# Performance work log

Measured on AMD Instinct MI355X. Metric: run time of the kernel, lower is better.

Reference implementation:

```python
import jax, jax.numpy as jnp
import numpy as np

NUM_HEADS = 8
TEMPERATURE = 10000.0


def sine_embed(pos, dim):
    """Sine positional embedding of 2D offsets. pos [..., 2] -> [..., dim]."""
    half = dim // 2  # dims per coordinate
    dim_t = TEMPERATURE ** (2.0 * (jnp.arange(half) // 2).astype(jnp.float32) / half)
    s = pos[..., :, None] / dim_t  # [..., 2, half]
    emb = jnp.stack([jnp.sin(s[..., 0::2]), jnp.cos(s[..., 1::2])], axis=-1)
    emb = emb.reshape(s.shape[:-1] + (half,))  # interleaved sin/cos per coord
    return emb.reshape(pos.shape[:-1] + (dim,))


def setup_inputs() -> dict:
    key = jax.random.key(0)
    ks = jax.random.split(key, 16)
    N, H, W, C, K = 2, 40, 40, 256, 100
    h = NUM_HEADS
    sc = 1.0 / np.sqrt(C)
    return {
        "query_feature": jax.random.normal(ks[0], (N, H, W, C), jnp.float32),
        "query_position": jax.random.uniform(ks[1], (N, H, W, 2), jnp.float32),
        "key_feature": jax.random.normal(ks[2], (N, K, C), jnp.float32),
        "key_position": jax.random.uniform(ks[3], (N, K, 2), jnp.float32),
        # MultiheadAttention params (torch convention: weight [out, in])
        "in_proj_w": jax.random.normal(ks[4], (3 * C, C), jnp.float32) * sc,
        "in_proj_b": jnp.zeros((3 * C,), jnp.float32),
        "out_proj_w": jax.random.normal(ks[5], (C, C), jnp.float32) * sc,
        "out_proj_b": jnp.zeros((C,), jnp.float32),
        # PositionalEncodingSineLearned MLP: sine(C) -> C -> num_heads
        "pos_w1": jax.random.normal(ks[6], (C, C), jnp.float32) * sc,
        "pos_b1": jnp.zeros((C,), jnp.float32),
        "pos_w2": jax.random.normal(ks[7], (h, C), jnp.float32) * sc,
        "pos_b2": jnp.zeros((h,), jnp.float32),
        # cat_pos branch params
        "pos_trans_w": jax.random.normal(ks[8], (2, 2), jnp.float32),
        "embed_w": jax.random.normal(ks[9], (C, C + 2), jnp.float32) * 0.01,
        "embed_b": jnp.zeros((C,), jnp.float32),
    }


def reference(query_feature, query_position, key_feature, key_position,
              in_proj_w, in_proj_b, out_proj_w, out_proj_b,
              pos_w1, pos_b1, pos_w2, pos_b2,
              pos_trans_w, embed_w, embed_b):
    N, H, W, C = query_feature.shape
    h = NUM_HEADS
    d = C // h
    q = query_feature.reshape(N, -1, C)            # [N,Q,C]
    qp = query_position.reshape(N, -1, 2)          # [N,Q,2] (scale_terms = 1.0)
    Q = q.shape[1]
    K = key_feature.shape[1]

    # pairwise relative positions: [N,Q,K,2]
    rel_pos = key_position[:, None, :, :] - qp[:, :, None, :]

    # learned sine relative positional encoding -> per-head additive bias
    pe = sine_embed(rel_pos, C)                              # [N,Q,K,C]
    hid = jax.nn.relu(pe @ pos_w1.T + pos_b1)                # [N,Q,K,C]
    bias = (hid @ pos_w2.T + pos_b2).transpose(0, 3, 1, 2)   # [N,h,Q,K]

    # multihead attention with additive relative bias
    wq, wk, wv = jnp.split(in_proj_w, 3, axis=0)
    bq, bk, bv = jnp.split(in_proj_b, 3, axis=0)
    qh = ((q @ wq.T + bq).reshape(N, Q, h, d)) * (d ** -0.5)
    kh = (key_feature @ wk.T + bk).reshape(N, K, h, d)
    vh = (key_feature @ wv.T + bv).reshape(N, K, h, d)
    scores = jnp.einsum('nqhd,nkhd->nhqk', qh, kh) + bias
    attn = jax.nn.softmax(scores, axis=-1)                   # [N,h,Q,K]
    ctx = jnp.einsum('nhqk,nkhd->nqhd', attn, vh).reshape(N, Q, C)
    refined = ctx @ out_proj_w.T + out_proj_b                # [N,Q,C]

    # cat_pos: attention-weighted relative position aggregation
    attn_w = attn.mean(axis=1)                               # [N,Q,K]
    new_rel = jnp.einsum('nqk,nqkc->nqc', attn_w, jax.lax.stop_gradient(rel_pos))
    new_pos = new_rel @ pos_trans_w.T                        # [N,Q,2]

    feat = jax.nn.relu(q + refined)
    feat = jax.nn.relu(jnp.concatenate([feat, new_pos], axis=-1) @ embed_w.T + embed_b)
    return feat.reshape(N, H, W, C)
```

## Files before the change

kernel.cpp:

```cpp
#include <hip/hip_runtime.h>
#include <math.h>

typedef __bf16 bf16x8 __attribute__((ext_vector_type(8)));
typedef __bf16 bf16x4 __attribute__((ext_vector_type(4)));
typedef float  f32x4  __attribute__((ext_vector_type(4)));

#define WS_KH    0u
#define WS_VH    51200u
#define WS_EWT   102400u
#define WS_OWT   168448u
#define WS_QHB   233984u
#define WS_BIASB 643584u
#define WS_KEB   1923584u
#define WS_W1B   1949984u
#define WS_W2PB  1982752u
#define WS_IPWT  1984800u

__device__ __forceinline__ float rdlane(float v, int l) {
  return __uint_as_float(__builtin_amdgcn_readlane(__float_as_uint(v), l));
}

__global__ __launch_bounds__(256) void prep1_kernel(
    const float* __restrict__ kpos,
    const float* __restrict__ pos_w1, const float* __restrict__ pos_w2,
    const float* __restrict__ embed_w, const float* __restrict__ out_w,
    const float* __restrict__ ipw, float* __restrict__ ws)
{
  __shared__ float tile[64 * 65];
  int bid = blockIdx.x, t = threadIdx.x;

  if (bid < 50) {
    int r = bid * 4 + (t >> 6);
    int u = t & 63;
    float p0 = kpos[r * 2 + 0], p1 = kpos[r * 2 + 1];
    __bf16* keb = (__bf16*)(ws + WS_KEB);
    bf16x4 o;
#pragma unroll
    for (int j = 0; j < 4; j++) {
      int col = u * 4 + j;
      int c = col >> 7, i = (col & 127) >> 1;
      float p = c ? p1 : p0;
      float inv = exp2f((float)i * (-13.287712379549449f / 64.0f));
      float v = p * inv;
      o[j] = (__bf16)((col & 1) ? __cosf(v) : __sinf(v));
    }
    *(bf16x4*)(keb + r * 264 + u * 4) = o;
  } else if (bid < 114) {
    int idx = (bid - 50) * 1024 + t * 4;
    float4 v = *(const float4*)(pos_w1 + idx);
    bf16x4 o; o[0] = (__bf16)v.x; o[1] = (__bf16)v.y; o[2] = (__bf16)v.z; o[3] = (__bf16)v.w;
    *(bf16x4*)((__bf16*)(ws + WS_W1B) + idx) = o;
  } else if (bid == 114) {
    __bf16* w2pb = (__bf16*)(ws + WS_W2PB);
    for (int i = 0; i < 16; i++) {
      int idx = t * 16 + i;
      w2pb[idx] = (idx < 2048) ? (__bf16)pos_w2[idx] : (__bf16)0.0f;
    }
  } else if (bid < 135) {
    int idx = bid - 115;
    int j0 = (idx / 4) * 64, c0 = (idx % 4) * 64;
    int jj = t & 63, rq = t >> 6;
    for (int rr = 0; rr < 16; rr++) {
      int c = rr * 4 + rq;
      float v = (j0 + jj < 258) ? embed_w[(c0 + c) * 258 + j0 + jj] : 0.0f;
      tile[c * 65 + jj] = v;
    }
    __syncthreads();
    int cc = t & 63, jq = t >> 6;
    for (int pp = 0; pp < 16; pp++) {
      int j = pp * 4 + jq;
      if (j0 + j < 258)
        ws[WS_EWT + (unsigned)(j0 + j) * 256u + c0 + cc] = tile[cc * 65 + j];
    }
  } else if (bid < 151) {
    int idx = bid - 135;
    int j0 = (idx >> 2) * 64, c0 = (idx & 3) * 64;
    int jj = t & 63, rq = t >> 6;
    for (int rr = 0; rr < 16; rr++) {
      int c = rr * 4 + rq;
      tile[c * 65 + jj] = out_w[(c0 + c) * 256 + j0 + jj];
    }
    __syncthreads();
    int cc = t & 63, jq = t >> 6;
    for (int pp = 0; pp < 16; pp++) {
      int j = pp * 4 + jq;
      ws[WS_OWT + (unsigned)(j0 + j) * 256u + c0 + cc] = tile[cc * 65 + j];
    }
  } else {
    int idx = bid - 151;
    int j0 = (idx & 3) * 64, o0 = (idx >> 2) * 64;
    int jj = t & 63, rq = t >> 6;
    for (int rr = 0; rr < 16; rr++) {
      int o = rr * 4 + rq;
      tile[o * 65 + jj] = ipw[(unsigned)(o0 + o) * 256u + j0 + jj];
    }
    __syncthreads();
    __bf16* ipwt = (__bf16*)(ws + WS_IPWT);
    int oo = t & 63, jq = t >> 6;
    for (int pp = 0; pp < 16; pp++) {
      int j = pp * 4 + jq;
      ipwt[(unsigned)(j0 + j) * 768u + o0 + oo] = (__bf16)tile[oo * 65 + j];
    }
  }
}

__global__ __launch_bounds__(256, 2) void prep2_kernel(
    const float* __restrict__ qfeat, const float* __restrict__ kfeat,
    const float* __restrict__ ipb, float* __restrict__ ws)
{
  __shared__ float x[8 * 256];
  int bid = blockIdx.x, t = threadIdx.x;
  const __bf16* ipwt = (const __bf16*)(ws + WS_IPWT);

  if (bid < 400) {
    int r0 = bid * 8;
    for (int i = t; i < 2048; i += 256) x[i] = qfeat[(unsigned)r0 * 256u + i];
    __syncthreads();
    float acc[8]; float bq = ipb[t];
#pragma unroll
    for (int rr = 0; rr < 8; rr++) acc[rr] = bq;
#pragma unroll 4
    for (int j = 0; j < 256; j += 4) {
      float w0 = (float)ipwt[(unsigned)(j + 0) * 768u + t];
      float w1 = (float)ipwt[(unsigned)(j + 1) * 768u + t];
      float w2 = (float)ipwt[(unsigned)(j + 2) * 768u + t];
      float w3 = (float)ipwt[(unsigned)(j + 3) * 768u + t];
#pragma unroll
      for (int rr = 0; rr < 8; rr++) {
        float4 x4 = *(const float4*)(x + rr * 256 + j);
        acc[rr] = fmaf(x4.x, w0, fmaf(x4.y, w1, fmaf(x4.z, w2, fmaf(x4.w, w3, acc[rr]))));
      }
    }
    __bf16* qhb = (__bf16*)(ws + WS_QHB);
#pragma unroll
    for (int rr = 0; rr < 8; rr++)
      qhb[(unsigned)(r0 + rr) * 256u + t] = (__bf16)(acc[rr] * 0.17677669529663687f);
  } else {
    int b2 = bid - 400; int n = b2 >> 4, tileI = b2 & 15;
    int r0l = tileI * 7; int cnt = 100 - r0l; if (cnt > 7) cnt = 7; if (cnt <= 0) return;
    int r0 = n * 100 + r0l;
    for (int i = t; i < cnt * 256; i += 256) x[i] = kfeat[(unsigned)r0 * 256u + i];
    __syncthreads();
    float ak[7], av[7]; float bk = ipb[256 + t], bv = ipb[512 + t];
#pragma unroll
    for (int rr = 0; rr < 7; rr++) { ak[rr] = bk; av[rr] = bv; }
#pragma unroll 2
    for (int j = 0; j < 256; j += 4) {
      float wk0 = (float)ipwt[(unsigned)(j + 0) * 768u + 256 + t];
      float wk1 = (float)ipwt[(unsigned)(j + 1) * 768u + 256 + t];
      float wk2 = (float)ipwt[(unsigned)(j + 2) * 768u + 256 + t];
      float wk3 = (float)ipwt[(unsigned)(j + 3) * 768u + 256 + t];
      float wv0 = (float)ipwt[(unsigned)(j + 0) * 768u + 512 + t];
      float wv1 = (float)ipwt[(unsigned)(j + 1) * 768u + 512 + t];
      float wv2 = (float)ipwt[(unsigned)(j + 2) * 768u + 512 + t];
      float wv3 = (float)ipwt[(unsigned)(j + 3) * 768u + 512 + t];
#pragma unroll
      for (int rr = 0; rr < 7; rr++) {
        float4 x4 = *(const float4*)(x + rr * 256 + j);
        ak[rr] = fmaf(x4.x, wk0, fmaf(x4.y, wk1, fmaf(x4.z, wk2, fmaf(x4.w, wk3, ak[rr]))));
        av[rr] = fmaf(x4.x, wv0, fmaf(x4.y, wv1, fmaf(x4.z, wv2, fmaf(x4.w, wv3, av[rr]))));
      }
    }
    for (int rr = 0; rr < 7; rr++) {
      if (rr < cnt) {
        ws[WS_KH + (unsigned)(r0 + rr) * 256u + t] = ak[rr];
        ws[WS_VH + (unsigned)(r0 + rr) * 256u + t] = av[rr];
      }
    }
  }
}

__global__ __launch_bounds__(512) void bias_kernel(
    const float* __restrict__ qpos,
    const float* __restrict__ pos_b1, const float* __restrict__ pos_b2,
    float* __restrict__ ws)
{
  __shared__ __align__(16) char smem[63488];
  __bf16* qe_s   = (__bf16*)(smem + 28672);
  __bf16* region = (__bf16*)(smem + 30720);

  int bid = blockIdx.x;
  int n = bid / 400;
  int q0 = bid * 4;
  int t = threadIdx.x;
  int lane = t & 63, w = t >> 6;
  int l15 = lane & 15, quad = lane >> 4;

  const __bf16* keb = (const __bf16*)(ws + WS_KEB) + (unsigned)(n * 100) * 264u;
  const __bf16* w1b = (const __bf16*)(ws + WS_W1B);
  const __bf16* w2pb = (const __bf16*)(ws + WS_W2PB);
  __bf16* biasb = (__bf16*)(ws + WS_BIASB);

  {
    int idx = t * 2;
    int q = idx >> 8, u = idx & 255;
    int c = u >> 7, i = (u & 127) >> 1;
    float p = qpos[(q0 + q) * 2 + c];
    float inv = exp2f((float)i * (-13.287712379549449f / 64.0f));
    float v = p * inv;
    qe_s[idx]     = (__bf16)__sinf(v);
    qe_s[idx + 1] = (__bf16)__cosf(v);
  }

  bf16x8 wfrag[2][8];
#pragma unroll
  for (int ct = 0; ct < 2; ct++)
#pragma unroll
    for (int kc = 0; kc < 8; kc++)
      wfrag[ct][kc] = *(const bf16x8*)(w1b + (unsigned)(w * 32 + ct * 16 + l15) * 256u + kc * 32 + quad * 8);
  float b1v[2][4];
#pragma unroll
  for (int ct = 0; ct < 2; ct++)
#pragma unroll
    for (int r = 0; r < 4; r++) b1v[ct][r] = pos_b1[w * 32 + ct * 16 + quad * 4 + r];
  float b2v[4];
#pragma unroll
  for (int r = 0; r < 4; r++) b2v[r] = pos_b2[(quad * 4 + r) & 7];

  bool gact = (t < 448);
  int gkey = t >> 2, gsub = t & 3;
  int gmt = gkey >> 4, gkl = gkey & 15;
  int gkcl = gsub >> 1, gqd0 = (gsub & 1) * 2;
  bf16x8 gk0, gk1, gq0, gq1;

  auto gen_load = [&](int q, int pair) {
    if (gact) {
      int cb = pair * 64 + gsub * 16;
      const __bf16* qp = qe_s + q * 256 + cb;
      gq0 = *(const bf16x8*)qp;
      gq1 = *(const bf16x8*)(qp + 8);
      if (gkey < 100) {
        const __bf16* kp = keb + (unsigned)gkey * 264u + cb;
        gk0 = *(const bf16x8*)kp;
        gk1 = *(const bf16x8*)(kp + 8);
      }
    }
  };
  auto gen_store = [&](int buf) {
    if (gact) {
      bf16x8 fr0, fr1;
      if (gkey < 100) {
#pragma unroll
        for (int jj = 0; jj < 4; jj++) {
          float sk = (float)gk0[2 * jj], ck = (float)gk0[2 * jj + 1];
          float sq = (float)gq0[2 * jj], cq = (float)gq0[2 * jj + 1];
          fr0[2 * jj]     = (__bf16)(sk * cq - ck * sq);
          fr0[2 * jj + 1] = (__bf16)(ck * cq + sk * sq);
          float sk1 = (float)gk1[2 * jj], ck1 = (float)gk1[2 * jj + 1];
          float sq1 = (float)gq1[2 * jj], cq1 = (float)gq1[2 * jj + 1];
          fr1[2 * jj]     = (__bf16)(sk1 * cq1 - ck1 * sq1);
          fr1[2 * jj + 1] = (__bf16)(ck1 * cq1 + sk1 * sq1);
        }
      } else {
#pragma unroll
        for (int jj = 0; jj < 8; jj++) { fr0[jj] = (__bf16)0.f; fr1[jj] = (__bf16)0.f; }
      }
      bf16x8* base = (bf16x8*)smem + buf * 896 + gkcl * 448 + gmt * 64;
      base[gqd0 * 16 + (gkl ^ (gqd0 * 2 + gkcl))]           = fr0;
      base[(gqd0 + 1) * 16 + (gkl ^ (gqd0 * 2 + 2 + gkcl))] = fr1;
    }
  };

  f32x4 zero4; zero4[0] = 0.f; zero4[1] = 0.f; zero4[2] = 0.f; zero4[3] = 0.f;

  __syncthreads();
  gen_load(0, 0);
  gen_store(0);
  __syncthreads();

  for (int q = 0; q < 4; q++) {
    f32x4 acc[2][7];
#pragma unroll
    for (int ct = 0; ct < 2; ct++)
#pragma unroll
      for (int mt = 0; mt < 7; mt++) acc[ct][mt] = zero4;

    for (int p = 0; p < 4; p++) {
      int nq = q, npair = p + 1, nbuf = (p + 1) & 1;
      bool have_next = true;
      if (p == 3) {
        if (q < 3) { nq = q + 1; npair = 0; nbuf = 0; }
        else have_next = false;
      }
      if (have_next) gen_load(nq, npair);

      const bf16x8* pb = (const bf16x8*)smem + (p & 1) * 896;
#pragma unroll
      for (int kh = 0; kh < 2; kh++) {
        int kc = p * 2 + kh;
        bf16x8 pf[7];
#pragma unroll
        for (int mt = 0; mt < 7; mt++)
          pf[mt] = pb[kh * 448 + mt * 64 + quad * 16 + (l15 ^ (quad * 2 + kh))];
#pragma unroll
        for (int mt = 0; mt < 7; mt++) {
          acc[0][mt] = __builtin_amdgcn_mfma_f32_16x16x32_bf16(wfrag[0][kc], pf[mt], acc[0][mt], 0, 0, 0);
          acc[1][mt] = __builtin_amdgcn_mfma_f32_16x16x32_bf16(wfrag[1][kc], pf[mt], acc[1][mt], 0, 0, 0);
        }
      }
      if (have_next) gen_store(nbuf);
      __syncthreads();
    }

#pragma unroll
    for (int ct = 0; ct < 2; ct++)
#pragma unroll
      for (int mt = 0; mt < 7; mt++)
#pragma unroll
        for (int r = 0; r < 4; r++)
          acc[ct][mt][r] = fmaxf(acc[ct][mt][r] + b1v[ct][r], 0.0f);

    auto wreg = [&](int mt, int slot) {
#pragma unroll
      for (int ct = 0; ct < 2; ct++) {
        int qt = ct * 2 + (quad >> 1);
        int j0 = (quad & 1) * 4;
        bf16x4 o;
#pragma unroll
        for (int r = 0; r < 4; r++) o[r] = (__bf16)acc[ct][mt][r];
        *(bf16x4*)(region + slot * 4096 + ((w * 64 + qt * 16 + l15) << 3) + j0) = o;
      }
    };
    auto g2 = [&](int mt, int slot) {
      f32x4 acc2 = zero4;
      const bf16x8* rg = (const bf16x8*)(region + slot * 4096);
#pragma unroll
      for (int s = 0; s < 8; s++) {
        bf16x8 w2f = *(const bf16x8*)(w2pb + (unsigned)l15 * 256u + s * 32 + quad * 8);
        bf16x8 hf = rg[s * 64 + lane];
        acc2 = __builtin_amdgcn_mfma_f32_16x16x32_bf16(w2f, hf, acc2, 0, 0, 0);
      }
      if (quad < 2) {
        int key = mt * 16 + l15;
        if (key < 100) {
          bf16x4 o;
#pragma unroll
          for (int r = 0; r < 4; r++) o[r] = (__bf16)(acc2[r] + b2v[r]);
          *(bf16x4*)(biasb + ((unsigned)(q0 + q) * 100u + key) * 8u + quad * 4) = o;
        }
      }
    };

    wreg(0, 0); wreg(1, 1); wreg(2, 2); wreg(3, 3);
    __syncthreads();
    if (w < 4) g2(w, w);
    __syncthreads();
    wreg(4, 0); wreg(5, 1); wreg(6, 2);
    __syncthreads();
    if (w < 3) g2(4 + w, w);
  }
}

__global__ __launch_bounds__(256, 4) void attn_kernel(
    const float* __restrict__ qfeat, const float* __restrict__ qpos,
    const float* __restrict__ kpos,
    const float* __restrict__ out_b, const float* __restrict__ embed_b,
    const float* __restrict__ ptw,
    const float* __restrict__ ws, float* __restrict__ out)
{
  __shared__ float qh_s[4 * 8 * 36];
  __shared__ float attn_s[4 * 8 * 116];
  __shared__ float ctx_s[4 * 264];
  __shared__ float cat_s[4 * 264];
  __shared__ float aw_s[4 * 104];

  int bid = blockIdx.x;
  int qg0 = bid * 4;
  int n = bid / 400;
  int t = threadIdx.x;

  const __bf16* qhb = (const __bf16*)(ws + WS_QHB);
  const __bf16* biasb = (const __bf16*)(ws + WS_BIASB);
  const float* kh = ws + WS_KH;
  const float* vh = ws + WS_VH;
  const float* owt = ws + WS_OWT;
  const float* ewt = ws + WS_EWT;

  for (int i = t; i < 1024; i += 256) {
    int q = i >> 8, c = i & 255;
    qh_s[(q * 8 + (c >> 5)) * 36 + (c & 31)] = (float)qhb[(unsigned)(qg0 + q) * 256u + c];
  }
  __syncthreads();

  for (int i = 0; i < 4; i++) {
    int p = t + i * 256;
    if (p < 800) {
      int k = p >> 3, h = p & 7;
      const float4* kf = (const float4*)(kh + (unsigned)(n * 100 + k) * 256u + h * 32);
      float4 kv[8];
#pragma unroll
      for (int dd = 0; dd < 8; dd++) kv[dd] = kf[dd];
#pragma unroll
      for (int q = 0; q < 4; q++) {
        const float4* qf = (const float4*)(qh_s + (q * 8 + h) * 36);
        float s = (float)biasb[((unsigned)(qg0 + q) * 100u + k) * 8u + h];
#pragma unroll
        for (int dd = 0; dd < 8; dd++) {
          float4 qv = qf[dd];
          s += kv[dd].x * qv.x + kv[dd].y * qv.y + kv[dd].z * qv.z + kv[dd].w * qv.w;
        }
        attn_s[(q * 8 + h) * 116 + k] = s;
      }
    }
  }
  __syncthreads();

  {
    int q = t >> 6, h = (t >> 3) & 7, j = t & 7;
    float* row = attn_s + (q * 8 + h) * 116;
    float mx = -1e30f;
    for (int k = j; k < 100; k += 8) mx = fmaxf(mx, row[k]);
    mx = fmaxf(mx, __shfl_xor(mx, 1, 8));
    mx = fmaxf(mx, __shfl_xor(mx, 2, 8));
    mx = fmaxf(mx, __shfl_xor(mx, 4, 8));
    float sum = 0.f;
    for (int k = j; k < 100; k += 8) { float e = __expf(row[k] - mx); row[k] = e; sum += e; }
    sum += __shfl_xor(sum, 1, 8);
    sum += __shfl_xor(sum, 2, 8);
    sum += __shfl_xor(sum, 4, 8);
    float inv = 1.0f / sum;
    for (int k = j; k < 100; k += 8) row[k] *= inv;
  }
  __syncthreads();

  for (int p = t; p < 416; p += 256) {
    int q = p / 104, k = p % 104;
    if (k < 100) {
      float s = 0.f;
#pragma unroll
      for (int h = 0; h < 8; h++) s += attn_s[(q * 8 + h) * 116 + k];
      aw_s[q * 104 + k] = s * 0.125f;
    }
  }
  {
    int c = t, h = c >> 5;
    float a0 = 0.f, a1 = 0.f, a2 = 0.f, a3 = 0.f;
    const float* vp = vh + (unsigned)(n * 100) * 256u + c;
    const float* r0 = attn_s + (0 * 8 + h) * 116;
    const float* r1 = attn_s + (1 * 8 + h) * 116;
    const float* r2 = attn_s + (2 * 8 + h) * 116;
    const float* r3 = attn_s + (3 * 8 + h) * 116;
#pragma unroll 4
    for (int k = 0; k < 100; k++) {
      float vv = vp[(unsigned)k * 256u];
      a0 = fmaf(r0[k], vv, a0);
      a1 = fmaf(r1[k], vv, a1);
      a2 = fmaf(r2[k], vv, a2);
      a3 = fmaf(r3[k], vv, a3);
    }
    ctx_s[0 * 264 + c] = a0; ctx_s[1 * 264 + c] = a1;
    ctx_s[2 * 264 + c] = a2; ctx_s[3 * 264 + c] = a3;
  }
  __syncthreads();

  if (t < 8) {
    int q = t >> 1, cd = t & 1;
    float qp = qpos[(qg0 + q) * 2 + cd];
    float s = 0.f;
    for (int k = 0; k < 100; k++)
      s = fmaf(aw_s[q * 104 + k], kpos[(n * 100 + k) * 2 + cd] - qp, s);
    float so = __shfl_xor(s, 1, 2);
    if (cd == 0) cat_s[q * 264 + 256] = ptw[0] * s + ptw[1] * so;
    else         cat_s[q * 264 + 257] = ptw[2] * so + ptw[3] * s;
  }

  {
    int c = t, lane = t & 63;
    float ob = out_b[c];
    float acc0 = ob, acc1 = ob, acc2 = ob, acc3 = ob;
    for (int ch = 0; ch < 4; ch++) {
      float v0 = ctx_s[0 * 264 + ch * 64 + lane];
      float v1 = ctx_s[1 * 264 + ch * 64 + lane];
      float v2 = ctx_s[2 * 264 + ch * 64 + lane];
      float v3 = ctx_s[3 * 264 + ch * 64 + lane];
      const float* wp = owt + (unsigned)(ch * 64) * 256u + c;
#pragma unroll 8
      for (int j2 = 0; j2 < 64; j2++) {
        float wv = wp[(unsigned)j2 * 256u];
        acc0 = fmaf(rdlane(v0, j2), wv, acc0);
        acc1 = fmaf(rdlane(v1, j2), wv, acc1);
        acc2 = fmaf(rdlane(v2, j2), wv, acc2);
        acc3 = fmaf(rdlane(v3, j2), wv, acc3);
      }
    }
    cat_s[0 * 264 + c] = fmaxf(qfeat[(unsigned)(qg0 + 0) * 256u + c] + acc0, 0.f);
    cat_s[1 * 264 + c] = fmaxf(qfeat[(unsigned)(qg0 + 1) * 256u + c] + acc1, 0.f);
    cat_s[2 * 264 + c] = fmaxf(qfeat[(unsigned)(qg0 + 2) * 256u + c] + acc2, 0.f);
    cat_s[3 * 264 + c] = fmaxf(qfeat[(unsigned)(qg0 + 3) * 256u + c] + acc3, 0.f);
  }
  __syncthreads();

  {
    int c = t, lane = t & 63;
    float eb = embed_b[c];
    float acc0 = eb, acc1 = eb, acc2 = eb, acc3 = eb;
    for (int ch = 0; ch < 4; ch++) {
      float v0 = cat_s[0 * 264 + ch * 64 + lane];
      float v1 = cat_s[1 * 264 + ch * 64 + lane];
      float v2 = cat_s[2 * 264 + ch * 64 + lane];
      float v3 = cat_s[3 * 264 + ch * 64 + lane];
      const float* wp = ewt + (unsigned)(ch * 64) * 256u + c;
#pragma unroll 8
      for (int j2 = 0; j2 < 64; j2++) {
        float wv = wp[(unsigned)j2 * 256u];
        acc0 = fmaf(rdlane(v0, j2), wv, acc0);
        acc1 = fmaf(rdlane(v1, j2), wv, acc1);
        acc2 = fmaf(rdlane(v2, j2), wv, acc2);
        acc3 = fmaf(rdlane(v3, j2), wv, acc3);
      }
    }
    float w256 = ewt[256u * 256u + c];
    float w257 = ewt[257u * 256u + c];
    acc0 += cat_s[0 * 264 + 256] * w256 + cat_s[0 * 264 + 257] * w257;
    acc1 += cat_s[1 * 264 + 256] * w256 + cat_s[1 * 264 + 257] * w257;
    acc2 += cat_s[2 * 264 + 256] * w256 + cat_s[2 * 264 + 257] * w257;
    acc3 += cat_s[3 * 264 + 256] * w256 + cat_s[3 * 264 + 257] * w257;
    out[(unsigned)(qg0 + 0) * 256u + c] = fmaxf(acc0, 0.f);
    out[(unsigned)(qg0 + 1) * 256u + c] = fmaxf(acc1, 0.f);
    out[(unsigned)(qg0 + 2) * 256u + c] = fmaxf(acc2, 0.f);
    out[(unsigned)(qg0 + 3) * 256u + c] = fmaxf(acc3, 0.f);
  }
}

extern "C" void kernel_launch(void* const* d_in, const int* in_sizes, int n_in,
                              void* d_out, int out_size, void* d_ws, size_t ws_size,
                              hipStream_t stream)
{
  const float* query_feature  = (const float*)d_in[0];
  const float* query_position = (const float*)d_in[1];
  const float* key_feature    = (const float*)d_in[2];
  const float* key_position   = (const float*)d_in[3];
  const float* in_proj_w      = (const float*)d_in[4];
  const float* in_proj_b      = (const float*)d_in[5];
  const float* out_proj_w     = (const float*)d_in[6];
  const float* out_proj_b     = (const float*)d_in[7];
  const float* pos_w1         = (const float*)d_in[8];
  const float* pos_b1         = (const float*)d_in[9];
  const float* pos_w2         = (const float*)d_in[10];
  const float* pos_b2         = (const float*)d_in[11];
  const float* pos_trans_w    = (const float*)d_in[12];
  const float* embed_w        = (const float*)d_in[13];
  const float* embed_b        = (const float*)d_in[14];
  float* ws  = (float*)d_ws;
  float* out = (float*)d_out;

  hipLaunchKernelGGL(prep1_kernel, dim3(199), dim3(256), 0, stream,
                     key_position, pos_w1, pos_w2, embed_w, out_proj_w,
                     in_proj_w, ws);
  hipLaunchKernelGGL(prep2_kernel, dim3(432), dim3(256), 0, stream,
                     query_feature, key_feature, in_proj_b, ws);
  hipLaunchKernelGGL(bias_kernel, dim3(800), dim3(512), 0, stream,
                     query_position, pos_b1, pos_b2, ws);
  hipLaunchKernelGGL(attn_kernel, dim3(800), dim3(256), 0, stream,
                     query_feature, query_position, key_position,
                     out_proj_b, embed_b, pos_trans_w,
                     ws, out);
}
```

Measured before the change: 299.7 us.

## Fuse positional bias MLP into attention kernel with one query per block

```diff
diff --git a/kernel.cpp b/kernel.cpp
--- a/kernel.cpp
+++ b/kernel.cpp
@@ -7,14 +7,13 @@
 
 #define WS_KH    0u
 #define WS_VH    51200u
-#define WS_EWT   102400u
-#define WS_OWT   168448u
-#define WS_QHB   233984u
-#define WS_BIASB 643584u
-#define WS_KEB   1923584u
-#define WS_W1B   1949984u
-#define WS_W2PB  1982752u
-#define WS_IPWT  1984800u
+#define WS_EWTB  102400u
+#define WS_OWTB  135424u
+#define WS_QHB   168192u
+#define WS_KEB   577792u
+#define WS_W1B   604192u
+#define WS_W2PB  636960u
+#define WS_IPWT  639008u
 
 __device__ __forceinline__ float rdlane(float v, int l) {
   return __uint_as_float(__builtin_amdgcn_readlane(__float_as_uint(v), l));
@@ -66,11 +65,12 @@
       tile[c * 65 + jj] = v;
     }
     __syncthreads();
+    __bf16* ewtb = (__bf16*)(ws + WS_EWTB);
     int cc = t & 63, jq = t >> 6;
     for (int pp = 0; pp < 16; pp++) {
       int j = pp * 4 + jq;
       if (j0 + j < 258)
-        ws[WS_EWT + (unsigned)(j0 + j) * 256u + c0 + cc] = tile[cc * 65 + j];
+        ewtb[(unsigned)(j0 + j) * 256u + c0 + cc] = (__bf16)tile[cc * 65 + j];
     }
   } else if (bid < 151) {
     int idx = bid - 135;
@@ -81,10 +81,11 @@
       tile[c * 65 + jj] = out_w[(c0 + c) * 256 + j0 + jj];
     }
     __syncthreads();
+    __bf16* owtb = (__bf16*)(ws + WS_OWTB);
     int cc = t & 63, jq = t >> 6;
     for (int pp = 0; pp < 16; pp++) {
       int j = pp * 4 + jq;
-      ws[WS_OWT + (unsigned)(j0 + j) * 256u + c0 + cc] = tile[cc * 65 + j];
+      owtb[(unsigned)(j0 + j) * 256u + c0 + cc] = (__bf16)tile[cc * 65 + j];
     }
   } else {
     int idx = bid - 151;
@@ -170,355 +171,254 @@
   }
 }
 
-__global__ __launch_bounds__(512) void bias_kernel(
-    const float* __restrict__ qpos,
+__global__ __launch_bounds__(256) void fused_kernel(
+    const float* __restrict__ qpos, const float* __restrict__ kpos,
+    const float* __restrict__ qfeat,
     const float* __restrict__ pos_b1, const float* __restrict__ pos_b2,
-    float* __restrict__ ws)
-{
-  __shared__ __align__(16) char smem[63488];
-  __bf16* qe_s   = (__bf16*)(smem + 28672);
-  __bf16* region = (__bf16*)(smem + 30720);
-
-  int bid = blockIdx.x;
-  int n = bid / 400;
-  int q0 = bid * 4;
-  int t = threadIdx.x;
-  int lane = t & 63, w = t >> 6;
-  int l15 = lane & 15, quad = lane >> 4;
-
-  const __bf16* keb = (const __bf16*)(ws + WS_KEB) + (unsigned)(n * 100) * 264u;
-  const __bf16* w1b = (const __bf16*)(ws + WS_W1B);
-  const __bf16* w2pb = (const __bf16*)(ws + WS_W2PB);
-  __bf16* biasb = (__bf16*)(ws + WS_BIASB);
-
-  {
-    int idx = t * 2;
-    int q = idx >> 8, u = idx & 255;
-    int c = u >> 7, i = (u & 127) >> 1;
-    float p = qpos[(q0 + q) * 2 + c];
-    float inv = exp2f((float)i * (-13.287712379549449f / 64.0f));
-    float v = p * inv;
-    qe_s[idx]     = (__bf16)__sinf(v);
-    qe_s[idx + 1] = (__bf16)__cosf(v);
-  }
-
-  bf16x8 wfrag[2][8];
-#pragma unroll
-  for (int ct = 0; ct < 2; ct++)
-#pragma unroll
-    for (int kc = 0; kc < 8; kc++)
-      wfrag[ct][kc] = *(const bf16x8*)(w1b + (unsigned)(w * 32 + ct * 16 + l15) * 256u + kc * 32 + quad * 8);
-  float b1v[2][4];
-#pragma unroll
-  for (int ct = 0; ct < 2; ct++)
-#pragma unroll
-    for (int r = 0; r < 4; r++) b1v[ct][r] = pos_b1[w * 32 + ct * 16 + quad * 4 + r];
-  float b2v[4];
-#pragma unroll
-  for (int r = 0; r < 4; r++) b2v[r] = pos_b2[(quad * 4 + r) & 7];
-
-  bool gact = (t < 448);
-  int gkey = t >> 2, gsub = t & 3;
-  int gmt = gkey >> 4, gkl = gkey & 15;
-  int gkcl = gsub >> 1, gqd0 = (gsub & 1) * 2;
-  bf16x8 gk0, gk1, gq0, gq1;
-
-  auto gen_load = [&](int q, int pair) {
-    if (gact) {
-      int cb = pair * 64 + gsub * 16;
-      const __bf16* qp = qe_s + q * 256 + cb;
-      gq0 = *(const bf16x8*)qp;
-      gq1 = *(const bf16x8*)(qp + 8);
-      if (gkey < 100) {
-        const __bf16* kp = keb + (unsigned)gkey * 264u + cb;
-        gk0 = *(const bf16x8*)kp;
-        gk1 = *(const bf16x8*)(kp + 8);
-      }
-    }
-  };
-  auto gen_store = [&](int buf) {
-    if (gact) {
-      bf16x8 fr0, fr1;
-      if (gkey < 100) {
-#pragma unroll
-        for (int jj = 0; jj < 4; jj++) {
-          float sk = (float)gk0[2 * jj], ck = (float)gk0[2 * jj + 1];
-          float sq = (float)gq0[2 * jj], cq = (float)gq0[2 * jj + 1];
-          fr0[2 * jj]     = (__bf16)(sk * cq - ck * sq);
-          fr0[2 * jj + 1] = (__bf16)(ck * cq + sk * sq);
-          float sk1 = (float)gk1[2 * jj], ck1 = (float)gk1[2 * jj + 1];
-          float sq1 = (float)gq1[2 * jj], cq1 = (float)gq1[2 * jj + 1];
-          fr1[2 * jj]     = (__bf16)(sk1 * cq1 - ck1 * sq1);
-          fr1[2 * jj + 1] = (__bf16)(ck1 * cq1 + sk1 * sq1);
-        }
-      } else {
-#pragma unroll
-        for (int jj = 0; jj < 8; jj++) { fr0[jj] = (__bf16)0.f; fr1[jj] = (__bf16)0.f; }
-      }
-      bf16x8* base = (bf16x8*)smem + buf * 896 + gkcl * 448 + gmt * 64;
-      base[gqd0 * 16 + (gkl ^ (gqd0 * 2 + gkcl))]           = fr0;
-      base[(gqd0 + 1) * 16 + (gkl ^ (gqd0 * 2 + 2 + gkcl))] = fr1;
-    }
-  };
-
-  f32x4 zero4; zero4[0] = 0.f; zero4[1] = 0.f; zero4[2] = 0.f; zero4[3] = 0.f;
-
-  __syncthreads();
-  gen_load(0, 0);
-  gen_store(0);
-  __syncthreads();
-
-  for (int q = 0; q < 4; q++) {
-    f32x4 acc[2][7];
-#pragma unroll
-    for (int ct = 0; ct < 2; ct++)
-#pragma unroll
-      for (int mt = 0; mt < 7; mt++) acc[ct][mt] = zero4;
-
-    for (int p = 0; p < 4; p++) {
-      int nq = q, npair = p + 1, nbuf = (p + 1) & 1;
-      bool have_next = true;
-      if (p == 3) {
-        if (q < 3) { nq = q + 1; npair = 0; nbuf = 0; }
-        else have_next = false;
-      }
-      if (have_next) gen_load(nq, npair);
-
-      const bf16x8* pb = (const bf16x8*)smem + (p & 1) * 896;
-#pragma unroll
-      for (int kh = 0; kh < 2; kh++) {
-        int kc = p * 2 + kh;
-        bf16x8 pf[7];
-#pragma unroll
-        for (int mt = 0; mt < 7; mt++)
-          pf[mt] = pb[kh * 448 + mt * 64 + quad * 16 + (l15 ^ (quad * 2 + kh))];
-#pragma unroll
-        for (int mt = 0; mt < 7; mt++) {
-          acc[0][mt] = __builtin_amdgcn_mfma_f32_16x16x32_bf16(wfrag[0][kc], pf[mt], acc[0][mt], 0, 0, 0);
-          acc[1][mt] = __builtin_amdgcn_mfma_f32_16x16x32_bf16(wfrag[1][kc], pf[mt], acc[1][mt], 0, 0, 0);
-        }
-      }
-      if (have_next) gen_store(nbuf);
-      __syncthreads();
-    }
-
-#pragma unroll
-    for (int ct = 0; ct < 2; ct++)
-#pragma unroll
-      for (int mt = 0; mt < 7; mt++)
-#pragma unroll
-        for (int r = 0; r < 4; r++)
-          acc[ct][mt][r] = fmaxf(acc[ct][mt][r] + b1v[ct][r], 0.0f);
-
-    auto wreg = [&](int mt, int slot) {
-#pragma unroll
-      for (int ct = 0; ct < 2; ct++) {
-        int qt = ct * 2 + (quad >> 1);
-        int j0 = (quad & 1) * 4;
-        bf16x4 o;
-#pragma unroll
-        for (int r = 0; r < 4; r++) o[r] = (__bf16)acc[ct][mt][r];
-        *(bf16x4*)(region + slot * 4096 + ((w * 64 + qt * 16 + l15) << 3) + j0) = o;
-      }
-    };
-    auto g2 = [&](int mt, int slot) {
-      f32x4 acc2 = zero4;
-      const bf16x8* rg = (const bf16x8*)(region + slot * 4096);
-#pragma unroll
-      for (int s = 0; s < 8; s++) {
-        bf16x8 w2f = *(const bf16x8*)(w2pb + (unsigned)l15 * 256u + s * 32 + quad * 8);
-        bf16x8 hf = rg[s * 64 + lane];
-        acc2 = __builtin_amdgcn_mfma_f32_16x16x32_bf16(w2f, hf, acc2, 0, 0, 0);
-      }
-      if (quad < 2) {
-        int key = mt * 16 + l15;
-        if (key < 100) {
-          bf16x4 o;
-#pragma unroll
-          for (int r = 0; r < 4; r++) o[r] = (__bf16)(acc2[r] + b2v[r]);
-          *(bf16x4*)(biasb + ((unsigned)(q0 + q) * 100u + key) * 8u + quad * 4) = o;
-        }
-      }
-    };
-
-    wreg(0, 0); wreg(1, 1); wreg(2, 2); wreg(3, 3);
-    __syncthreads();
-    if (w < 4) g2(w, w);
-    __syncthreads();
-    wreg(4, 0); wreg(5, 1); wreg(6, 2);
-    __syncthreads();
-    if (w < 3) g2(4 + w, w);
-  }
-}
-
-__global__ __launch_bounds__(256, 4) void attn_kernel(
-    const float* __restrict__ qfeat, const float* __restrict__ qpos,
-    const float* __restrict__ kpos,
     const float* __restrict__ out_b, const float* __restrict__ embed_b,
     const float* __restrict__ ptw,
     const float* __restrict__ ws, float* __restrict__ out)
 {
-  __shared__ float qh_s[4 * 8 * 36];
-  __shared__ float attn_s[4 * 8 * 116];
-  __shared__ float ctx_s[4 * 264];
-  __shared__ float cat_s[4 * 264];
-  __shared__ float aw_s[4 * 104];
-
-  int bid = blockIdx.x;
-  int qg0 = bid * 4;
-  int n = bid / 400;
+  __shared__ __align__(16) char smem[40256];
+  __bf16* qe_s   = (__bf16*)smem;
+  __bf16* region = (__bf16*)(smem + 512);
+  float* attn_s  = (float*)(smem + 33280);
+  float* qh_s    = (float*)(smem + 36608);
+  float* ctx_s   = (float*)(smem + 37760);
+  float* cat_s   = (float*)(smem + 38784);
+  float* aw_s    = (float*)(smem + 39840);
+
+  int q = blockIdx.x;
+  int n = q >> 11 ? 1 : (q >= 1600 ? 1 : 0);
+  n = (q >= 1600) ? 1 : 0;
   int t = threadIdx.x;
-
-  const __bf16* qhb = (const __bf16*)(ws + WS_QHB);
-  const __bf16* biasb = (const __bf16*)(ws + WS_BIASB);
+  int lane = t & 63, w = t >> 6;
+  int l15 = lane & 15, quad = lane >> 4;
+
+  const __bf16* keb  = (const __bf16*)(ws + WS_KEB) + (unsigned)(n * 100) * 264u;
+  const __bf16* w1b  = (const __bf16*)(ws + WS_W1B);
+  const __bf16* w2pb = (const __bf16*)(ws + WS_W2PB);
+  const __bf16* qhb  = (const __bf16*)(ws + WS_QHB);
   const float* kh = ws + WS_KH;
   const float* vh = ws + WS_VH;
-  const float* owt = ws + WS_OWT;
-  const float* ewt = ws + WS_EWT;
-
-  for (int i = t; i < 1024; i += 256) {
-    int q = i >> 8, c = i & 255;
-    qh_s[(q * 8 + (c >> 5)) * 36 + (c & 31)] = (float)qhb[(unsigned)(qg0 + q) * 256u + c];
-  }
-  __syncthreads();
-
+  const __bf16* owtb = (const __bf16*)(ws + WS_OWTB);
+  const __bf16* ewtb = (const __bf16*)(ws + WS_EWTB);
+
+  {
+    int c = t >> 7, i = (t & 127) >> 1;
+    float p = qpos[q * 2 + c];
+    float inv = exp2f((float)i * (-13.287712379549449f / 64.0f));
+    float v = p * inv;
+    qe_s[t] = (__bf16)((t & 1) ? __cosf(v) : __sinf(v));
+  }
+
+  float b1v[4][4];
+#pragma unroll
+  for (int ct = 0; ct < 4; ct++)
+#pragma unroll
+    for (int r = 0; r < 4; r++) b1v[ct][r] = pos_b1[w * 64 + ct * 16 + quad * 4 + r];
+  float b2v[4];
+#pragma unroll
+  for (int r = 0; r < 4; r++) b2v[r] = pos_b2[(quad * 4 + r) & 7];
+
+  f32x4 zero4; zero4[0] = 0.f; zero4[1] = 0.f; zero4[2] = 0.f; zero4[3] = 0.f;
+  f32x4 acc[4][7];
+#pragma unroll
+  for (int ct = 0; ct < 4; ct++)
+#pragma unroll
+    for (int mt = 0; mt < 7; mt++) acc[ct][mt] = zero4;
+
+  __syncthreads();
+
+  const __bf16* w1r = w1b + (unsigned)(w * 64 + l15) * 256u + quad * 8;
+  for (int kc = 0; kc < 8; kc++) {
+    bf16x8 wf[4];
+#pragma unroll
+    for (int ct = 0; ct < 4; ct++)
+      wf[ct] = *(const bf16x8*)(w1r + (unsigned)(ct * 16) * 256u + kc * 32);
+    bf16x8 qf = *(const bf16x8*)(qe_s + kc * 32 + quad * 8);
+    const __bf16* kebk = keb + kc * 32 + quad * 8;
+#pragma unroll
+    for (int mt = 0; mt < 7; mt++) {
+      int key = mt * 16 + l15;
+      bf16x8 bfr;
+      if (key < 100) {
+        bf16x8 kf = *(const bf16x8*)(kebk + (unsigned)key * 264u);
+#pragma unroll
+        for (int pp = 0; pp < 4; pp++) {
+          float sk = (float)kf[2 * pp], ck = (float)kf[2 * pp + 1];
+          float sq = (float)qf[2 * pp], cq = (float)qf[2 * pp + 1];
+          bfr[2 * pp]     = (__bf16)(sk * cq - ck * sq);
+          bfr[2 * pp + 1] = (__bf16)(ck * cq + sk * sq);
+        }
+      } else {
+#pragma unroll
+        for (int jj = 0; jj < 8; jj++) bfr[jj] = (__bf16)0.f;
+      }
+#pragma unroll
+      for (int ct = 0; ct < 4; ct++)
+        acc[ct][mt] = __builtin_amdgcn_mfma_f32_16x16x32_bf16(wf[ct], bfr, acc[ct][mt], 0, 0, 0);
+    }
+  }
+
+#pragma unroll
+  for (int ct = 0; ct < 4; ct++)
+#pragma unroll
+    for (int mt = 0; mt < 7; mt++)
+#pragma unroll
+      for (int r = 0; r < 4; r++)
+        acc[ct][mt][r] = fmaxf(acc[ct][mt][r] + b1v[ct][r], 0.0f);
+
+  auto swz = [](int row) { return row ^ ((row >> 4) & 7); };
+  auto wreg = [&](int mt, int slot) {
+#pragma unroll
+    for (int ct = 0; ct < 4; ct++) {
+      int row = (2 * w + (ct >> 1)) * 64 + ((ct & 1) * 2 + (quad >> 1)) * 16 + l15;
+      int r2 = swz(row);
+      bf16x4 o;
+#pragma unroll
+      for (int r = 0; r < 4; r++) o[r] = (__bf16)acc[ct][mt][r];
+      *(bf16x4*)(region + slot * 4096 + r2 * 8 + (quad & 1) * 4) = o;
+    }
+  };
+  auto g2 = [&](int mt, int slot) {
+    f32x4 acc2 = zero4;
+    const __bf16* rg = region + slot * 4096;
+#pragma unroll
+    for (int s = 0; s < 8; s++) {
+      bf16x8 w2f = *(const bf16x8*)(w2pb + (unsigned)l15 * 256u + s * 32 + quad * 8);
+      int row = s * 64 + lane;
+      bf16x8 hf = *(const bf16x8*)(rg + swz(row) * 8);
+      acc2 = __builtin_amdgcn_mfma_f32_16x16x32_bf16(w2f, hf, acc2, 0, 0, 0);
+    }
+    if (quad < 2) {
+      int key = mt * 16 + l15;
+      if (key < 100) {
+#pragma unroll
+        for (int r = 0; r < 4; r++)
+          attn_s[(quad * 4 + r) * 104 + key] = acc2[r] + b2v[r];
+      }
+    }
+  };
+
+  wreg(0, 0); wreg(1, 1); wreg(2, 2); wreg(3, 3);
+  __syncthreads();
+  g2(w, w);
+  __syncthreads();
+  wreg(4, 0); wreg(5, 1); wreg(6, 2);
+  __syncthreads();
+  if (w < 3) {
+    g2(4 + w, w);
+  } else {
+    bf16x4 v4 = *(const bf16x4*)(qhb + (unsigned)q * 256u + lane * 4);
+    int c = lane * 4;
+    float* dst = qh_s + (c >> 5) * 36 + (c & 31);
+    dst[0] = (float)v4[0]; dst[1] = (float)v4[1];
+    dst[2] = (float)v4[2]; dst[3] = (float)v4[3];
+  }
+  __syncthreads();
+
+#pragma unroll
   for (int i = 0; i < 4; i++) {
     int p = t + i * 256;
     if (p < 800) {
       int k = p >> 3, h = p & 7;
-      const float4* kf = (const float4*)(kh + (unsigned)(n * 100 + k) * 256u + h * 32);
-      float4 kv[8];
-#pragma unroll
-      for (int dd = 0; dd < 8; dd++) kv[dd] = kf[dd];
-#pragma unroll
-      for (int q = 0; q < 4; q++) {
-        const float4* qf = (const float4*)(qh_s + (q * 8 + h) * 36);
-        float s = (float)biasb[((unsigned)(qg0 + q) * 100u + k) * 8u + h];
-#pragma unroll
-        for (int dd = 0; dd < 8; dd++) {
-          float4 qv = qf[dd];
-          s += kv[dd].x * qv.x + kv[dd].y * qv.y + kv[dd].z * qv.z + kv[dd].w * qv.w;
-        }
-        attn_s[(q * 8 + h) * 116 + k] = s;
-      }
+      const float4* kf4 = (const float4*)(kh + (unsigned)(n * 100 + k) * 256u + h * 32);
+      const float4* qf4 = (const float4*)(qh_s + h * 36);
+      float s = attn_s[h * 104 + k];
+#pragma unroll
+      for (int dd = 0; dd < 8; dd++) {
+        float4 kv = kf4[dd], qv = qf4[dd];
+        s += kv.x * qv.x + kv.y * qv.y + kv.z * qv.z + kv.w * qv.w;
+      }
+      attn_s[h * 104 + k] = s;
     }
   }
   __syncthreads();
 
   {
-    int q = t >> 6, h = (t >> 3) & 7, j = t & 7;
-    float* row = attn_s + (q * 8 + h) * 116;
+    int h = t >> 5, j = t & 31;
+    float* row = attn_s + h * 104;
     float mx = -1e30f;
-    for (int k = j; k < 100; k += 8) mx = fmaxf(mx, row[k]);
-    mx = fmaxf(mx, __shfl_xor(mx, 1, 8));
-    mx = fmaxf(mx, __shfl_xor(mx, 2, 8));
-    mx = fmaxf(mx, __shfl_xor(mx, 4, 8));
+    for (int k = j; k < 100; k += 32) mx = fmaxf(mx, row[k]);
+    mx = fmaxf(mx, __shfl_xor(mx, 1, 32));
+    mx = fmaxf(mx, __shfl_xor(mx, 2, 32));
+    mx = fmaxf(mx, __shfl_xor(mx, 4, 32));
+    mx = fmaxf(mx, __shfl_xor(mx, 8, 32));
+    mx = fmaxf(mx, __shfl_xor(mx, 16, 32));
     float sum = 0.f;
-    for (int k = j; k < 100; k += 8) { float e = __expf(row[k] - mx); row[k] = e; sum += e; }
-    sum += __shfl_xor(sum, 1, 8);
-    sum += __shfl_xor(sum, 2, 8);
-    sum += __shfl_xor(sum, 4, 8);
+    for (int k = j; k < 100; k += 32) { float e = __expf(row[k] - mx); row[k] = e; sum += e; }
+    sum += __shfl_xor(sum, 1, 32);
+    sum += __shfl_xor(sum, 2, 32);
+    sum += __shfl_xor(sum, 4, 32);
+    sum += __shfl_xor(sum, 8, 32);
+    sum += __shfl_xor(sum, 16, 32);
     float inv = 1.0f / sum;
-    for (int k = j; k < 100; k += 8) row[k] *= inv;
-  }
-  __syncthreads();
-
-  for (int p = t; p < 416; p += 256) {
-    int q = p / 104, k = p % 104;
-    if (k < 100) {
-      float s = 0.f;
-#pragma unroll
-      for (int h = 0; h < 8; h++) s += attn_s[(q * 8 + h) * 116 + k];
-      aw_s[q * 104 + k] = s * 0.125f;
-    }
+    for (int k = j; k < 100; k += 32) row[k] *= inv;
+  }
+  __syncthreads();
+
+  if (t < 100) {
+    float s = 0.f;
+#pragma unroll
+    for (int h = 0; h < 8; h++) s += attn_s[h * 104 + t];
+    aw_s[t] = s * 0.125f;
   }
   {
     int c = t, h = c >> 5;
-    float a0 = 0.f, a1 = 0.f, a2 = 0.f, a3 = 0.f;
+    float a = 0.f;
     const float* vp = vh + (unsigned)(n * 100) * 256u + c;
-    const float* r0 = attn_s + (0 * 8 + h) * 116;
-    const float* r1 = attn_s + (1 * 8 + h) * 116;
-    const float* r2 = attn_s + (2 * 8 + h) * 116;
-    const float* r3 = attn_s + (3 * 8 + h) * 116;
+    const float* rw = attn_s + h * 104;
 #pragma unroll 4
-    for (int k = 0; k < 100; k++) {
-      float vv = vp[(unsigned)k * 256u];
-      a0 = fmaf(r0[k], vv, a0);
-      a1 = fmaf(r1[k], vv, a1);
-      a2 = fmaf(r2[k], vv, a2);
-      a3 = fmaf(r3[k], vv, a3);
-    }
-    ctx_s[0 * 264 + c] = a0; ctx_s[1 * 264 + c] = a1;
-    ctx_s[2 * 264 + c] = a2; ctx_s[3 * 264 + c] = a3;
-  }
-  __syncthreads();
-
-  if (t < 8) {
-    int q = t >> 1, cd = t & 1;
-    float qp = qpos[(qg0 + q) * 2 + cd];
+    for (int k = 0; k < 100; k++)
+      a = fmaf(rw[k], vp[(unsigned)k * 256u], a);
+    ctx_s[c] = a;
+  }
+  __syncthreads();
+
+  if (t < 2) {
+    int cd = t;
+    float qp = qpos[q * 2 + cd];
     float s = 0.f;
     for (int k = 0; k < 100; k++)
-      s = fmaf(aw_s[q * 104 + k], kpos[(n * 100 + k) * 2 + cd] - qp, s);
+      s = fmaf(aw_s[k], kpos[(n * 100 + k) * 2 + cd] - qp, s);
     float so = __shfl_xor(s, 1, 2);
-    if (cd == 0) cat_s[q * 264 + 256] = ptw[0] * s + ptw[1] * so;
-    else         cat_s[q * 264 + 257] = ptw[2] * so + ptw[3] * s;
+    if (cd == 0) cat_s[256] = ptw[0] * s + ptw[1] * so;
+    else         cat_s[257] = ptw[2] * so + ptw[3] * s;
   }
 
   {
-    int c = t, lane = t & 63;
-    float ob = out_b[c];
-    float acc0 = ob, acc1 = ob, acc2 = ob, acc3 = ob;
+    int c = t;
+    float acc0 = out_b[c];
     for (int ch = 0; ch < 4; ch++) {
-      float v0 = ctx_s[0 * 264 + ch * 64 + lane];
-      float v1 = ctx_s[1 * 264 + ch * 64 + lane];
-      float v2 = ctx_s[2 * 264 + ch * 64 + lane];
-      float v3 = ctx_s[3 * 264 + ch * 64 + lane];
-      const float* wp = owt + (unsigned)(ch * 64) * 256u + c;
+      float v0 = ctx_s[ch * 64 + lane];
+      const __bf16* wp = owtb + (unsigned)(ch * 64) * 256u + c;
 #pragma unroll 8
       for (int j2 = 0; j2 < 64; j2++) {
-        float wv = wp[(unsigned)j2 * 256u];
+        float wv = (float)wp[(unsigned)j2 * 256u];
         acc0 = fmaf(rdlane(v0, j2), wv, acc0);
-        acc1 = fmaf(rdlane(v1, j2), wv, acc1);
-        acc2 = fmaf(rdlane(v2, j2), wv, acc2);
-        acc3 = fmaf(rdlane(v3, j2), wv, acc3);
-      }
-    }
-    cat_s[0 * 264 + c] = fmaxf(qfeat[(unsigned)(qg0 + 0) * 256u + c] + acc0, 0.f);
-    cat_s[1 * 264 + c] = fmaxf(qfeat[(unsigned)(qg0 + 1) * 256u + c] + acc1, 0.f);
-    cat_s[2 * 264 + c] = fmaxf(qfeat[(unsigned)(qg0 + 2) * 256u + c] + acc2, 0.f);
-    cat_s[3 * 264 + c] = fmaxf(qfeat[(unsigned)(qg0 + 3) * 256u + c] + acc3, 0.f);
+      }
+    }
+    cat_s[c] = fmaxf(qfeat[(unsigned)q * 256u + c] + acc0, 0.f);
   }
   __syncthreads();
 
   {
-    int c = t, lane = t & 63;
-    float eb = embed_b[c];
-    float acc0 = eb, acc1 = eb, acc2 = eb, acc3 = eb;
+    int c = t;
+    float acc0 = embed_b[c];
     for (int ch = 0; ch < 4; ch++) {
-      float v0 = cat_s[0 * 264 + ch * 64 + lane];
-      float v1 = cat_s[1 * 264 + ch * 64 + lane];
-      float v2 = cat_s[2 * 264 + ch * 64 + lane];
-      float v3 = cat_s[3 * 264 + ch * 64 + lane];
-      const float* wp = ewt + (unsigned)(ch * 64) * 256u + c;
+      float v0 = cat_s[ch * 64 + lane];
+      const __bf16* wp = ewtb + (unsigned)(ch * 64) * 256u + c;
 #pragma unroll 8
       for (int j2 = 0; j2 < 64; j2++) {
-        float wv = wp[(unsigned)j2 * 256u];
+        float wv = (float)wp[(unsigned)j2 * 256u];
         acc0 = fmaf(rdlane(v0, j2), wv, acc0);
-        acc1 = fmaf(rdlane(v1, j2), wv, acc1);
-        acc2 = fmaf(rdlane(v2, j2), wv, acc2);
-        acc3 = fmaf(rdlane(v3, j2), wv, acc3);
-      }
-    }
-    float w256 = ewt[256u * 256u + c];
-    float w257 = ewt[257u * 256u + c];
-    acc0 += cat_s[0 * 264 + 256] * w256 + cat_s[0 * 264 + 257] * w257;
-    acc1 += cat_s[1 * 264 + 256] * w256 + cat_s[1 * 264 + 257] * w257;
-    acc2 += cat_s[2 * 264 + 256] * w256 + cat_s[2 * 264 + 257] * w257;
-    acc3 += cat_s[3 * 264 + 256] * w256 + cat_s[3 * 264 + 257] * w257;
-    out[(unsigned)(qg0 + 0) * 256u + c] = fmaxf(acc0, 0.f);
-    out[(unsigned)(qg0 + 1) * 256u + c] = fmaxf(acc1, 0.f);
-    out[(unsigned)(qg0 + 2) * 256u + c] = fmaxf(acc2, 0.f);
-    out[(unsigned)(qg0 + 3) * 256u + c] = fmaxf(acc3, 0.f);
+      }
+    }
+    float w256 = (float)ewtb[256u * 256u + c];
+    float w257 = (float)ewtb[257u * 256u + c];
+    acc0 += cat_s[256] * w256 + cat_s[257] * w257;
+    out[(unsigned)q * 256u + c] = fmaxf(acc0, 0.f);
   }
 }
 
@@ -549,10 +449,8 @@
                      in_proj_w, ws);
   hipLaunchKernelGGL(prep2_kernel, dim3(432), dim3(256), 0, stream,
                      query_feature, key_feature, in_proj_b, ws);
-  hipLaunchKernelGGL(bias_kernel, dim3(800), dim3(512), 0, stream,
-                     query_position, pos_b1, pos_b2, ws);
-  hipLaunchKernelGGL(attn_kernel, dim3(800), dim3(256), 0, stream,
-                     query_feature, query_position, key_position,
-                     out_proj_b, embed_b, pos_trans_w,
+  hipLaunchKernelGGL(fused_kernel, dim3(3200), dim3(256), 0, stream,
+                     query_position, key_position, query_feature,
+                     pos_b1, pos_b2, out_proj_b, embed_b, pos_trans_w,
                      ws, out);
 }
```

After: 591.7 us. +97.4%, slower.
